# Kernel optimization log

Measured on AMD Instinct MI355X. Metric: run time of the kernel, lower is better.

## Reference

```python
import jax, jax.numpy as jnp
import numpy as np

ALPHA = 0.2  # LeakyReLU negative slope
NEG = -1e10  # mask value, matches -10000000000.0


def _gat_head(feat, adj, W, a1, a2):
    # feat: [N, Fin], W: [Fin, Fout], a1/a2: [Fout]
    h = feat @ W                              # [N, Fout]
    s = h @ a1                                # [N] attn_for_self
    t = h @ a2                                # [N] attn_for_neighs
    logits = jax.nn.leaky_relu(s[:, None] + t[None, :], ALPHA)  # [N, N]
    logits = logits + NEG * (1.0 - adj)       # additive adjacency mask
    attn = jax.nn.softmax(logits, axis=-1)    # [N, N]
    return attn @ h                           # [N, Fout]


def setup_inputs() -> dict:
    key = jax.random.key(0)
    ks = jax.random.split(key, 9)
    N, NFEAT, NHID, NCLASS, H = 6144, 128, 64, 16, 4
    glorot = jax.nn.initializers.glorot_uniform()
    adj = (jax.random.uniform(ks[0], (N, N)) < 0.005).astype(jnp.float32)
    feature = jax.random.normal(ks[1], (N, NFEAT), dtype=jnp.float32)
    in0 = NFEAT * H
    W0 = jnp.stack([glorot(ks[2 + i], (in0, NHID), jnp.float32) for i in range(H)])  # [H,in0,NHID]
    a1_0 = jax.random.normal(ks[6], (H, NHID), dtype=jnp.float32) * 0.1
    a2_0 = jax.random.normal(ks[7], (H, NHID), dtype=jnp.float32) * 0.1
    Wout = glorot(ks[8], (NHID * H, NCLASS), jnp.float32)
    a1_out = jax.random.normal(jax.random.fold_in(key, 100), (NCLASS,), dtype=jnp.float32) * 0.1
    a2_out = jax.random.normal(jax.random.fold_in(key, 101), (NCLASS,), dtype=jnp.float32) * 0.1
    return {"adj": adj, "feature": feature, "W0": W0, "a1_0": a1_0, "a2_0": a2_0,
            "Wout": Wout, "a1_out": a1_out, "a2_out": a2_out}


def reference(adj, feature, W0, a1_0, a2_0, Wout, a1_out, a2_out):
    H = W0.shape[0]
    N = feature.shape[0]
    x = jnp.tile(feature, (1, H))  # [N, nfeat*H]
    # hidden layer: H heads, concat=True -> elu then concat along features
    heads = jax.vmap(_gat_head, in_axes=(None, None, 0, 0, 0))(x, adj, W0, a1_0, a2_0)  # [H,N,NHID]
    heads = jax.nn.elu(heads)
    x = jnp.transpose(heads, (1, 0, 2)).reshape(N, -1)  # [N, H*NHID]
    # output layer: concat=False (no elu inside), then elu + softmax in GAT.call
    out = _gat_head(x, adj, Wout, a1_out, a2_out)  # [N, nclass]
    out = jax.nn.elu(out)
    return jax.nn.softmax(out, axis=-1)
```

## Files before the change

kernel.cpp:

```cpp
#include <hip/hip_runtime.h>
#include <cstdint>
#include <math.h>

#define N 6144
#define FIN 128
#define FH 64
#define NHEADS 4
#define NC 16
#define CAP 512
#define ALPHA 0.2f
#define NT 16

__device__ __forceinline__ float wave_sum(float v) {
    #pragma unroll
    for (int off = 32; off >= 1; off >>= 1) v += __shfl_xor(v, off);
    return v;
}
__device__ __forceinline__ float wave_max(float v) {
    #pragma unroll
    for (int off = 32; off >= 1; off >>= 1) v = fmaxf(v, __shfl_xor(v, off));
    return v;
}

__global__ void k_reduce_w(const float* __restrict__ W0, float* __restrict__ weff) {
    int idx = blockIdx.x * 256 + threadIdx.x;
    if (idx >= NHEADS * FIN * FH) return;
    int f = idx & 63, k = (idx >> 6) & 127, h = idx >> 13;
    const float* base = W0 + (size_t)h * 512 * 64;
    float s = 0.f;
    #pragma unroll
    for (int r = 0; r < 4; r++) s += base[(size_t)(r * 128 + k) * 64 + f];
    weff[idx] = s;
}

__global__ void k_hgemm(const float* __restrict__ feat, const float* __restrict__ weff,
                        const float* __restrict__ a1, const float* __restrict__ a2,
                        float* __restrict__ hfeat, float* __restrict__ sb,
                        float* __restrict__ tb) {
    __shared__ float fl[NT * FIN];
    int tid = threadIdx.x;
    int n0 = blockIdx.x * NT;
    for (int idx = tid; idx < NT * FIN; idx += 256) fl[idx] = feat[(size_t)n0 * FIN + idx];
    __syncthreads();
    int f = tid & 63, h = tid >> 6;
    const float* wcol = weff + (size_t)h * FIN * FH + f;
    float acc[NT];
    #pragma unroll
    for (int nn = 0; nn < NT; nn++) acc[nn] = 0.f;
    for (int k = 0; k < FIN; k++) {
        float w = wcol[(size_t)k * FH];
        #pragma unroll
        for (int nn = 0; nn < NT; nn++) acc[nn] = fmaf(fl[nn * FIN + k], w, acc[nn]);
    }
    float a1v = a1[h * FH + f], a2v = a2[h * FH + f];
    #pragma unroll
    for (int nn = 0; nn < NT; nn++) {
        hfeat[((size_t)h * N + (n0 + nn)) * FH + f] = acc[nn];
        float s = wave_sum(acc[nn] * a1v);
        float t = wave_sum(acc[nn] * a2v);
        if ((tid & 63) == 0) {
            sb[h * N + n0 + nn] = s;
            tb[h * N + n0 + nn] = t;
        }
    }
}

__global__ void k_row(const float* __restrict__ adj, const float* __restrict__ hfeat,
                      const float* __restrict__ sb, const float* __restrict__ tb,
                      int* __restrict__ cols, int* __restrict__ deg,
                      float* __restrict__ x1) {
    int i = blockIdx.x;
    int tid = threadIdx.x;
    int lane = tid & 63, h = tid >> 6;
    __shared__ int lidx[CAP];
    __shared__ int cnt;
    if (tid == 0) cnt = 0;
    __syncthreads();

    const float4* rowv = (const float4*)(adj + (size_t)i * N);
    unsigned long long lmask = (1ull << lane) - 1ull;
    #pragma unroll
    for (int it = 0; it < N / 1024; it++) {
        int v = it * 256 + tid;
        float4 rv = rowv[v];
        int jb = 4 * v;
        bool p[4] = {rv.x != 0.f, rv.y != 0.f, rv.z != 0.f, rv.w != 0.f};
        #pragma unroll
        for (int c = 0; c < 4; c++) {
            unsigned long long m = __ballot(p[c]);
            int tot = __popcll(m);
            if (tot) {
                int prefix = __popcll(m & lmask);
                int wb;
                if (lane == 0) wb = atomicAdd(&cnt, tot);
                wb = __shfl(wb, 0);
                int pos = wb + prefix;
                if (p[c] && pos < CAP) lidx[pos] = jb + c;
            }
        }
    }
    __syncthreads();
    int d = cnt;
    if (tid == 0) deg[i] = d;
    for (int t = tid; t < min(d, CAP); t += 256) cols[(size_t)i * CAP + t] = lidx[t];

    int mode = (d == 0) ? 1 : (d > CAP ? 2 : 0);
    int count = (mode == 0) ? d : N;
    const float* trow = tb + (size_t)h * N;
    const float* hrow = hfeat + (size_t)h * N * FH;
    float si = sb[h * N + i];
    int q = lane >> 4, fo = (lane & 15) * 4;
    float m = -INFINITY, l = 0.f;
    float4 acc = {0.f, 0.f, 0.f, 0.f};
    for (int base = 0; base < count; base += 64) {
        int idx = base + lane;
        int j = 0; float lr = -INFINITY;
        if (idx < count) {
            j = (mode == 0) ? lidx[idx] : idx;
            bool ok = (mode != 2) || (adj[(size_t)i * N + j] != 0.f);
            if (ok) {
                float z = si + trow[j];
                lr = (z >= 0.f) ? z : ALPHA * z;
            }
        }
        float mc = wave_max(lr);
        float mn = fmaxf(m, mc);
        if (mn == -INFINITY) continue;
        float scale = (m == -INFINITY) ? 0.f : expf(m - mn);
        float w = (lr == -INFINITY) ? 0.f : expf(lr - mn);
        l = l * scale + wave_sum(w);
        acc.x *= scale; acc.y *= scale; acc.z *= scale; acc.w *= scale;
        int cn = min(64, count - base);
        #pragma unroll 4
        for (int b = 0; b < cn; b += 4) {
            float wb = __shfl(w, b + q);
            int jn = __shfl(j, b + q);
            float4 hv = *(const float4*)(hrow + (size_t)jn * FH + fo);
            acc.x = fmaf(wb, hv.x, acc.x);
            acc.y = fmaf(wb, hv.y, acc.y);
            acc.z = fmaf(wb, hv.z, acc.z);
            acc.w = fmaf(wb, hv.w, acc.w);
        }
        m = mn;
    }
    #pragma unroll
    for (int off = 16; off <= 32; off <<= 1) {
        acc.x += __shfl_xor(acc.x, off);
        acc.y += __shfl_xor(acc.y, off);
        acc.z += __shfl_xor(acc.z, off);
        acc.w += __shfl_xor(acc.w, off);
    }
    if (lane < 16) {
        float linv = 1.f / l;
        float4 o;
        o.x = acc.x * linv; o.y = acc.y * linv; o.z = acc.z * linv; o.w = acc.w * linv;
        o.x = (o.x > 0.f) ? o.x : expm1f(o.x);
        o.y = (o.y > 0.f) ? o.y : expm1f(o.y);
        o.z = (o.z > 0.f) ? o.z : expm1f(o.z);
        o.w = (o.w > 0.f) ? o.w : expm1f(o.w);
        *(float4*)(x1 + (size_t)i * (NHEADS * FH) + h * FH + fo) = o;
    }
}

__global__ void k_ogemm(const float* __restrict__ x1, const float* __restrict__ wout,
                        const float* __restrict__ a1o, const float* __restrict__ a2o,
                        float* __restrict__ h2, float* __restrict__ s2,
                        float* __restrict__ t2) {
    int w = threadIdx.x >> 6, lane = threadIdx.x & 63;
    int n = blockIdx.x * 4 + w;
    int f = lane & 15, part = lane >> 4;
    const float* xr = x1 + (size_t)n * 256 + part * 64;
    float dot = 0.f;
    for (int k = 0; k < 64; k++) dot = fmaf(xr[k], wout[(size_t)(part * 64 + k) * NC + f], dot);
    dot += __shfl_xor(dot, 16);
    dot += __shfl_xor(dot, 32);
    if (lane < NC) h2[(size_t)n * NC + lane] = dot;
    float sv = (lane < NC) ? dot * a1o[lane] : 0.f;
    float tv = (lane < NC) ? dot * a2o[lane] : 0.f;
    sv = wave_sum(sv); tv = wave_sum(tv);
    if (lane == 0) { s2[n] = sv; t2[n] = tv; }
}

__global__ void k_attn_out(const float* __restrict__ h2, const float* __restrict__ s2,
                           const float* __restrict__ t2, const int* __restrict__ cols,
                           const int* __restrict__ deg, const float* __restrict__ adj,
                           float* __restrict__ out) {
    int w = threadIdx.x >> 6, lane = threadIdx.x & 63;
    int i = blockIdx.x * 4 + w;
    int d = deg[i];
    int mode = (d == 0) ? 1 : (d > CAP ? 2 : 0);
    int count = (mode == 0) ? d : N;
    const int* crow = cols + (size_t)i * CAP;
    float si = s2[i];
    int f = lane & 15, q = lane >> 4;
    float m = -INFINITY, l = 0.f, acc = 0.f;
    for (int base = 0; base < count; base += 64) {
        int idx = base + lane;
        int j = 0; float lr = -INFINITY;
        if (idx < count) {
            j = (mode == 0) ? crow[idx] : idx;
            bool ok = (mode != 2) || (adj[(size_t)i * N + j] != 0.f);
            if (ok) {
                float z = si + t2[j];
                lr = (z >= 0.f) ? z : ALPHA * z;
            }
        }
        float mc = wave_max(lr);
        float mn = fmaxf(m, mc);
        if (mn == -INFINITY) continue;
        float scale = (m == -INFINITY) ? 0.f : expf(m - mn);
        float wv = (lr == -INFINITY) ? 0.f : expf(lr - mn);
        l = l * scale + wave_sum(wv);
        acc *= scale;
        int cn = min(64, count - base);
        #pragma unroll 4
        for (int b = 0; b < cn; b += 4) {
            float wb = __shfl(wv, b + q);
            int jn = __shfl(j, b + q);
            acc = fmaf(wb, h2[(size_t)jn * NC + f], acc);
        }
        m = mn;
    }
    acc += __shfl_xor(acc, 16);
    acc += __shfl_xor(acc, 32);
    float o = acc / l;
    o = (o > 0.f) ? o : expm1f(o);
    float mv = (lane < NC) ? o : -INFINITY;
    float mx = wave_max(mv);
    float e = (lane < NC) ? expf(o - mx) : 0.f;
    float se = wave_sum(e);
    if (lane < NC) out[(size_t)i * NC + lane] = e / se;
}

extern "C" void kernel_launch(void* const* d_in, const int* in_sizes, int n_in,
                              void* d_out, int out_size, void* d_ws, size_t ws_size,
                              hipStream_t stream) {
    const float* adj  = (const float*)d_in[0];
    const float* feat = (const float*)d_in[1];
    const float* W0   = (const float*)d_in[2];
    const float* a1_0 = (const float*)d_in[3];
    const float* a2_0 = (const float*)d_in[4];
    const float* Wout = (const float*)d_in[5];
    const float* a1o  = (const float*)d_in[6];
    const float* a2o  = (const float*)d_in[7];
    float* out = (float*)d_out;

    float* weff  = (float*)d_ws;
    float* hfeat = weff + 32768;
    float* sb    = hfeat + 1572864;
    float* tb    = sb + 24576;
    float* x1    = tb + 24576;
    float* h2    = x1 + 1572864;
    float* s2    = h2 + 98304;
    float* t2    = s2 + 6144;
    int*   cols  = (int*)(t2 + 6144);
    int*   deg   = cols + (size_t)N * CAP;

    k_reduce_w<<<128, 256, 0, stream>>>(W0, weff);
    k_hgemm<<<N / NT, 256, 0, stream>>>(feat, weff, a1_0, a2_0, hfeat, sb, tb);
    k_row<<<N, 256, 0, stream>>>(adj, hfeat, sb, tb, cols, deg, x1);
    k_ogemm<<<N / 4, 256, 0, stream>>>(x1, Wout, a1o, a2o, h2, s2, t2);
    k_attn_out<<<N / 4, 256, 0, stream>>>(h2, s2, t2, cols, deg, adj, out);
}
```

Before: 279.2 us.

## Fuse output-layer projection into row attention kernel and batch adjacency loads

Removes the separate k_ogemm kernel. Each k_row block now keeps its ELU'd hidden row in shared memory, and one wave computes the output-layer projection plus the s2/t2 scores from it. This drops the x1 global write and re-read and one kernel launch. It also hoists all six float4 adjacency loads ahead of the ballot compaction loop so the memory requests are in flight together. The cost is an extra barrier, a serial 64-step dot product on one wave per block, and more registers held for the prefetched loads.

```diff
diff --git a/kernel.cpp b/kernel.cpp
--- a/kernel.cpp
+++ b/kernel.cpp
@@ -67,30 +67,35 @@
 
 __global__ void k_row(const float* __restrict__ adj, const float* __restrict__ hfeat,
                       const float* __restrict__ sb, const float* __restrict__ tb,
+                      const float* __restrict__ wout, const float* __restrict__ a1o,
+                      const float* __restrict__ a2o,
                       int* __restrict__ cols, int* __restrict__ deg,
-                      float* __restrict__ x1) {
+                      float* __restrict__ h2, float* __restrict__ s2,
+                      float* __restrict__ t2) {
     int i = blockIdx.x;
     int tid = threadIdx.x;
     int lane = tid & 63, h = tid >> 6;
     __shared__ int lidx[CAP];
+    __shared__ float xrow[NHEADS * FH];
     __shared__ int cnt;
     if (tid == 0) cnt = 0;
     __syncthreads();
 
     const float4* rowv = (const float4*)(adj + (size_t)i * N);
+    float4 rv[6];
+    #pragma unroll
+    for (int it = 0; it < 6; it++) rv[it] = rowv[it * 256 + tid];
     unsigned long long lmask = (1ull << lane) - 1ull;
     #pragma unroll
-    for (int it = 0; it < N / 1024; it++) {
-        int v = it * 256 + tid;
-        float4 rv = rowv[v];
-        int jb = 4 * v;
-        bool p[4] = {rv.x != 0.f, rv.y != 0.f, rv.z != 0.f, rv.w != 0.f};
+    for (int it = 0; it < 6; it++) {
+        int jb = (it * 256 + tid) * 4;
+        bool p[4] = {rv[it].x != 0.f, rv[it].y != 0.f, rv[it].z != 0.f, rv[it].w != 0.f};
         #pragma unroll
         for (int c = 0; c < 4; c++) {
-            unsigned long long m = __ballot(p[c]);
-            int tot = __popcll(m);
+            unsigned long long mm = __ballot(p[c]);
+            int tot = __popcll(mm);
             if (tot) {
-                int prefix = __popcll(m & lmask);
+                int prefix = __popcll(mm & lmask);
                 int wb;
                 if (lane == 0) wb = atomicAdd(&cnt, tot);
                 wb = __shfl(wb, 0);
@@ -158,27 +163,24 @@
         o.y = (o.y > 0.f) ? o.y : expm1f(o.y);
         o.z = (o.z > 0.f) ? o.z : expm1f(o.z);
         o.w = (o.w > 0.f) ? o.w : expm1f(o.w);
-        *(float4*)(x1 + (size_t)i * (NHEADS * FH) + h * FH + fo) = o;
-    }
-}
-
-__global__ void k_ogemm(const float* __restrict__ x1, const float* __restrict__ wout,
-                        const float* __restrict__ a1o, const float* __restrict__ a2o,
-                        float* __restrict__ h2, float* __restrict__ s2,
-                        float* __restrict__ t2) {
-    int w = threadIdx.x >> 6, lane = threadIdx.x & 63;
-    int n = blockIdx.x * 4 + w;
-    int f = lane & 15, part = lane >> 4;
-    const float* xr = x1 + (size_t)n * 256 + part * 64;
-    float dot = 0.f;
-    for (int k = 0; k < 64; k++) dot = fmaf(xr[k], wout[(size_t)(part * 64 + k) * NC + f], dot);
-    dot += __shfl_xor(dot, 16);
-    dot += __shfl_xor(dot, 32);
-    if (lane < NC) h2[(size_t)n * NC + lane] = dot;
-    float sv = (lane < NC) ? dot * a1o[lane] : 0.f;
-    float tv = (lane < NC) ? dot * a2o[lane] : 0.f;
-    sv = wave_sum(sv); tv = wave_sum(tv);
-    if (lane == 0) { s2[n] = sv; t2[n] = tv; }
+        *(float4*)(xrow + h * FH + fo) = o;
+    }
+    __syncthreads();
+
+    if (h == 0) {
+        int f = lane & 15, part = lane >> 4;
+        float dot = 0.f;
+        #pragma unroll
+        for (int k = 0; k < 64; k++)
+            dot = fmaf(xrow[part * 64 + k], wout[(size_t)(part * 64 + k) * NC + f], dot);
+        dot += __shfl_xor(dot, 16);
+        dot += __shfl_xor(dot, 32);
+        if (lane < NC) h2[(size_t)i * NC + lane] = dot;
+        float sv = (lane < NC) ? dot * a1o[lane] : 0.f;
+        float tv = (lane < NC) ? dot * a2o[lane] : 0.f;
+        sv = wave_sum(sv); tv = wave_sum(tv);
+        if (lane == 0) { s2[i] = sv; t2[i] = tv; }
+    }
 }
 
 __global__ void k_attn_out(const float* __restrict__ h2, const float* __restrict__ s2,
@@ -249,8 +251,7 @@
     float* hfeat = weff + 32768;
     float* sb    = hfeat + 1572864;
     float* tb    = sb + 24576;
-    float* x1    = tb + 24576;
-    float* h2    = x1 + 1572864;
+    float* h2    = tb + 24576;
     float* s2    = h2 + 98304;
     float* t2    = s2 + 6144;
     int*   cols  = (int*)(t2 + 6144);
@@ -258,7 +259,7 @@
 
     k_reduce_w<<<128, 256, 0, stream>>>(W0, weff);
     k_hgemm<<<N / NT, 256, 0, stream>>>(feat, weff, a1_0, a2_0, hfeat, sb, tb);
-    k_row<<<N, 256, 0, stream>>>(adj, hfeat, sb, tb, cols, deg, x1);
-    k_ogemm<<<N / 4, 256, 0, stream>>>(x1, Wout, a1o, a2o, h2, s2, t2);
+    k_row<<<N, 256, 0, stream>>>(adj, hfeat, sb, tb, Wout, a1o, a2o,
+                                 cols, deg, h2, s2, t2);
     k_attn_out<<<N / 4, 256, 0, stream>>>(h2, s2, t2, cols, deg, adj, out);
 }
```

New measurement: 261.6 us. 1.07x faster.
